# Optimization experiments

Hardware: AMD Instinct MI355X
Metric: run time of the kernel (lower is better)

Reference implementation:

```python
import jax, jax.numpy as jnp
import numpy as np


def setup_inputs() -> dict:
    key = jax.random.key(0)
    k1, k2, k3, k4 = jax.random.split(key, 4)
    T, IN, OUT = 4096, 4096, 4096  # tokens, in_features, out_features
    x = jax.random.normal(k1, (T, IN), dtype=jnp.float32)
    # simulated FP8 weight values (already quantized integers-ish codes stored as float)
    weight = jax.random.normal(k2, (OUT, IN), dtype=jnp.float32)
    # per-output-channel dequant scale
    weight_scale = jax.random.uniform(k3, (OUT,), dtype=jnp.float32, minval=0.01, maxval=0.1)
    bias = jax.random.normal(k4, (OUT,), dtype=jnp.float32)
    return {"x": x, "weight": weight, "weight_scale": weight_scale, "bias": bias}


def reference(x, weight, weight_scale, bias) -> jnp.ndarray:
    # FP8 quantized linear: dequantize weight with per-channel scale, then GEMM + bias.
    # weight: [out, in], weight_scale: [out], x: [tokens, in] -> out: [tokens, out]
    w_deq = weight * weight_scale[:, None]
    return jnp.einsum("ti,oi->to", x, w_deq) + bias
```

## Files before the change

### kernel.cpp

```cpp
#include <hip/hip_runtime.h>
#include <hip/hip_bf16.h>
#include <stdint.h>

typedef __bf16 bf16_t;
typedef bf16_t bf16x8 __attribute__((ext_vector_type(8)));
typedef float f32x4 __attribute__((ext_vector_type(4)));

#define BM 256
#define BN 256
#define BK 64

__device__ __forceinline__ void gload_lds16(const void* g, void* l) {
  __builtin_amdgcn_global_load_lds(
      (const __attribute__((address_space(1))) uint32_t*)g,
      (__attribute__((address_space(3))) uint32_t*)l, 16, 0, 0);
}

__global__ __launch_bounds__(256) void cvt_x_kernel(
    const float* __restrict__ in, bf16_t* __restrict__ out, int n8) {
  int stride = gridDim.x * blockDim.x;
  for (int i = blockIdx.x * blockDim.x + threadIdx.x; i < n8; i += stride) {
    const f32x4* p = (const f32x4*)in + 2 * (size_t)i;
    f32x4 a = p[0], b = p[1];
    bf16x8 o;
#pragma unroll
    for (int r = 0; r < 4; ++r) { o[r] = (bf16_t)a[r]; o[r + 4] = (bf16_t)b[r]; }
    *((bf16x8*)out + i) = o;
  }
}

__global__ __launch_bounds__(256) void cvt_w_kernel(
    const float* __restrict__ in, const float* __restrict__ scale,
    bf16_t* __restrict__ out, int k8, int n8) {
  int stride = gridDim.x * blockDim.x;
  for (int i = blockIdx.x * blockDim.x + threadIdx.x; i < n8; i += stride) {
    int row = i / k8;
    float s = scale[row];
    const f32x4* p = (const f32x4*)in + 2 * (size_t)i;
    f32x4 a = p[0], b = p[1];
    bf16x8 o;
#pragma unroll
    for (int r = 0; r < 4; ++r) {
      o[r] = (bf16_t)(a[r] * s);
      o[r + 4] = (bf16_t)(b[r] * s);
    }
    *((bf16x8*)out + i) = o;
  }
}

__global__ __launch_bounds__(512, 2) void gemm256(
    const bf16_t* __restrict__ A, const bf16_t* __restrict__ B,
    const float* __restrict__ bias, float* __restrict__ C,
    int M, int N, int K) {
  __shared__ __attribute__((aligned(16))) char lds[131072];

  const int tid = threadIdx.x;
  const int lane = tid & 63;
  const int wave = tid >> 6;
  const int wm = wave >> 2;
  const int wn = wave & 3;

  int nwg = gridDim.x;
  int wg = blockIdx.x;
  if ((nwg & 7) == 0) { int cpx = nwg >> 3; wg = (wg & 7) * cpx + (wg >> 3); }
  const int ntn = N / BN;
  const int tm = wg / ntn;
  const int tn = wg % ntn;

  const size_t Kb = (size_t)K * 2;
  const char* gApan = (const char*)A + (size_t)tm * BM * Kb;
  const char* gBpan = (const char*)B + (size_t)tn * BN * Kb;

  const int xc = (((lane >> 4) ^ (lane & 3)) << 4);
  int aoff[2][4], boff[4];
#pragma unroll
  for (int ch = 0; ch < 2; ++ch)
#pragma unroll
    for (int i = 0; i < 4; ++i) {
      int row = wm * 128 + ch * 64 + i * 16 + (lane & 15);
      aoff[ch][i] = row * 64 + xc;
    }
#pragma unroll
  for (int j = 0; j < 4; ++j) {
    int row = wn * 64 + j * 16 + (lane & 15);
    boff[j] = row * 64 + xc;
  }

  size_t srcoff[2];
  int ldst[2];
#pragma unroll
  for (int s = 0; s < 2; ++s) {
    int r = (wave * 2 + s) * 16 + (lane >> 2);
    int c = (lane & 3) ^ (r & 3);
    srcoff[s] = (size_t)r * Kb + (size_t)(c << 4);
    ldst[s] = (wave * 2 + s) * 1024;
  }

#define STAGE_U(dstbase, pan, kbyte)                                          \
  {                                                                           \
    gload_lds16((pan) + srcoff[0] + (size_t)(kbyte), lds + (dstbase) + ldst[0]); \
    gload_lds16((pan) + srcoff[1] + (size_t)(kbyte), lds + (dstbase) + ldst[1]); \
  }

  f32x4 acc[8][4];
#pragma unroll
  for (int a = 0; a < 8; ++a)
#pragma unroll
    for (int j = 0; j < 4; ++j) acc[a][j] = (f32x4)0.0f;

  const int NT = K / BK;

  STAGE_U(0,             gApan, 0);
  STAGE_U(32768,         gBpan, 0);
  STAGE_U(16384,         gApan, 64);
  STAGE_U(49152,         gBpan, 64);
  if (NT > 1) {
    STAGE_U(65536,         gApan, 128);
    STAGE_U(65536 + 32768, gBpan, 128);
    asm volatile("s_waitcnt vmcnt(4)" ::: "memory");
  } else {
    asm volatile("s_waitcnt vmcnt(0)" ::: "memory");
  }
  __builtin_amdgcn_s_barrier();

  for (int t = 0; t < NT; ++t) {
    const int bb = (t & 1) << 16;
    const int nb = bb ^ 65536;
    const size_t kb1 = (size_t)(t + 1) * 128;
    const size_t kb2 = (size_t)(t + 2) * 128;
    const bool st1 = (t + 1) < NT;
    const bool st2 = (t + 2) < NT;

    const char* lA0 = lds + bb;
    const char* lA1 = lds + bb + 16384;
    const char* lB0 = lds + bb + 32768;
    const char* lB1 = lds + bb + 49152;

    bf16x8 af[4], bf0[4], bf1[4];

#pragma unroll
    for (int i = 0; i < 4; ++i) af[i] = *(const bf16x8*)(lA0 + aoff[0][i]);
#pragma unroll
    for (int j = 0; j < 4; ++j) bf0[j] = *(const bf16x8*)(lB0 + boff[j]);
    if (st1) STAGE_U(nb + 16384, gApan, kb1 + 64);
    __builtin_amdgcn_s_barrier();
    asm volatile("s_waitcnt lgkmcnt(0)" ::: "memory");
    __builtin_amdgcn_s_setprio(1);
#pragma unroll
    for (int i = 0; i < 4; ++i)
#pragma unroll
      for (int j = 0; j < 4; ++j)
        acc[i][j] = __builtin_amdgcn_mfma_f32_16x16x32_bf16(af[i], bf0[j],
                                                            acc[i][j], 0, 0, 0);
    __builtin_amdgcn_s_setprio(0);
    __builtin_amdgcn_s_barrier();

#pragma unroll
    for (int i = 0; i < 4; ++i) af[i] = *(const bf16x8*)(lA0 + aoff[1][i]);
    if (st1) STAGE_U(nb + 49152, gBpan, kb1 + 64);
    __builtin_amdgcn_s_barrier();
    asm volatile("s_waitcnt lgkmcnt(0)" ::: "memory");
    __builtin_amdgcn_s_setprio(1);
#pragma unroll
    for (int i = 0; i < 4; ++i)
#pragma unroll
      for (int j = 0; j < 4; ++j)
        acc[4 + i][j] = __builtin_amdgcn_mfma_f32_16x16x32_bf16(
            af[i], bf0[j], acc[4 + i][j], 0, 0, 0);
    __builtin_amdgcn_s_setprio(0);
    __builtin_amdgcn_s_barrier();

#pragma unroll
    for (int i = 0; i < 4; ++i) af[i] = *(const bf16x8*)(lA1 + aoff[0][i]);
#pragma unroll
    for (int j = 0; j < 4; ++j) bf1[j] = *(const bf16x8*)(lB1 + boff[j]);
    if (st2) STAGE_U(bb, gApan, kb2);
    __builtin_amdgcn_s_barrier();
    asm volatile("s_waitcnt lgkmcnt(0)" ::: "memory");
    __builtin_amdgcn_s_setprio(1);
#pragma unroll
    for (int i = 0; i < 4; ++i)
#pragma unroll
      for (int j = 0; j < 4; ++j)
        acc[i][j] = __builtin_amdgcn_mfma_f32_16x16x32_bf16(af[i], bf1[j],
                                                            acc[i][j], 0, 0, 0);
    __builtin_amdgcn_s_setprio(0);
    __builtin_amdgcn_s_barrier();

#pragma unroll
    for (int i = 0; i < 4; ++i) af[i] = *(const bf16x8*)(lA1 + aoff[1][i]);
    if (st2) STAGE_U(bb + 32768, gBpan, kb2);
    __builtin_amdgcn_s_barrier();
    asm volatile("s_waitcnt lgkmcnt(0)" ::: "memory");
    __builtin_amdgcn_s_setprio(1);
#pragma unroll
    for (int i = 0; i < 4; ++i)
#pragma unroll
      for (int j = 0; j < 4; ++j)
        acc[4 + i][j] = __builtin_amdgcn_mfma_f32_16x16x32_bf16(
            af[i], bf1[j], acc[4 + i][j], 0, 0, 0);
    __builtin_amdgcn_s_setprio(0);
    if (st2)      asm volatile("s_waitcnt vmcnt(4)" ::: "memory");
    else if (st1) asm volatile("s_waitcnt vmcnt(0)" ::: "memory");
    __builtin_amdgcn_s_barrier();
  }
#undef STAGE_U

  const int row0 = tm * BM + wm * 128;
  const int col0 = tn * BN + wn * 64;
#pragma unroll
  for (int j = 0; j < 4; ++j) {
    int c = col0 + j * 16 + (lane & 15);
    float bv = bias[c];
#pragma unroll
    for (int a = 0; a < 8; ++a) {
      int ch = a >> 2, i = a & 3;
      int rbase = row0 + ch * 64 + i * 16 + ((lane >> 4) << 2);
#pragma unroll
      for (int r = 0; r < 4; ++r)
        C[(size_t)(rbase + r) * N + c] = acc[a][j][r] + bv;
    }
  }
}

__global__ void fallback_gemm(const float* __restrict__ x,
                              const float* __restrict__ w,
                              const float* __restrict__ s,
                              const float* __restrict__ b,
                              float* __restrict__ out, int M, int N, int K) {
  int o = blockIdx.x * blockDim.x + threadIdx.x;
  if (o >= M * N) return;
  int m = o / N, n = o % N;
  const float* xr = x + (size_t)m * K;
  const float* wr = w + (size_t)n * K;
  float acc = 0.f;
  for (int k = 0; k < K; ++k) acc += xr[k] * wr[k];
  out[o] = acc * s[n] + b[n];
}

extern "C" void kernel_launch(void* const* d_in, const int* in_sizes, int n_in,
                              void* d_out, int out_size, void* d_ws,
                              size_t ws_size, hipStream_t stream) {
  const float* x = (const float*)d_in[0];
  const float* w = (const float*)d_in[1];
  const float* sc = (const float*)d_in[2];
  const float* bias = (const float*)d_in[3];
  float* out = (float*)d_out;

  const int N = in_sizes[2];
  const int K = in_sizes[1] / N;
  const int M = in_sizes[0] / K;

  const size_t need = ((size_t)M * K + (size_t)N * K) * sizeof(bf16_t);
  const bool fast = (ws_size >= need) && (M % BM == 0) && (N % BN == 0) &&
                    (K % BK == 0) && (K / BK >= 1);

  if (fast) {
    bf16_t* xb = (bf16_t*)d_ws;
    bf16_t* wb = xb + (size_t)M * K;

    int n8x = (M * K) / 8;
    int n8w = (N * K) / 8;
    cvt_x_kernel<<<2048, 256, 0, stream>>>(x, xb, n8x);
    cvt_w_kernel<<<2048, 256, 0, stream>>>(w, sc, wb, K / 8, n8w);

    dim3 grid((M / BM) * (N / BN));
    gemm256<<<grid, 512, 0, stream>>>(xb, wb, bias, out, M, N, K);
  } else {
    int total = M * N;
    fallback_gemm<<<(total + 255) / 256, 256, 0, stream>>>(x, w, sc, bias, out,
                                                           M, N, K);
  }
}
```

Measured before the change: 167.5 us.

## Merge conversion kernels into one launch and change LDS swizzle pattern

Fuses the x and weight fp32-to-bf16 conversion kernels into a single launch, with block ranges split between the two jobs, removing one kernel launch and the gap between launches. It also changes the XOR swizzle used for LDS tile layout, both the global-to-LDS write column permutation and the matching read offsets, aiming to reduce LDS bank conflicts on the MFMA operand reads. The swizzle must stay consistent between writer and reader, so a mismatch would corrupt results.

```diff
diff --git a/kernel.cpp b/kernel.cpp
--- a/kernel.cpp
+++ b/kernel.cpp
@@ -16,35 +16,36 @@
       (__attribute__((address_space(3))) uint32_t*)l, 16, 0, 0);
 }
 
-__global__ __launch_bounds__(256) void cvt_x_kernel(
-    const float* __restrict__ in, bf16_t* __restrict__ out, int n8) {
-  int stride = gridDim.x * blockDim.x;
-  for (int i = blockIdx.x * blockDim.x + threadIdx.x; i < n8; i += stride) {
-    const f32x4* p = (const f32x4*)in + 2 * (size_t)i;
-    f32x4 a = p[0], b = p[1];
-    bf16x8 o;
-#pragma unroll
-    for (int r = 0; r < 4; ++r) { o[r] = (bf16_t)a[r]; o[r + 4] = (bf16_t)b[r]; }
-    *((bf16x8*)out + i) = o;
-  }
-}
-
-__global__ __launch_bounds__(256) void cvt_w_kernel(
-    const float* __restrict__ in, const float* __restrict__ scale,
-    bf16_t* __restrict__ out, int k8, int n8) {
-  int stride = gridDim.x * blockDim.x;
-  for (int i = blockIdx.x * blockDim.x + threadIdx.x; i < n8; i += stride) {
-    int row = i / k8;
-    float s = scale[row];
-    const f32x4* p = (const f32x4*)in + 2 * (size_t)i;
-    f32x4 a = p[0], b = p[1];
-    bf16x8 o;
-#pragma unroll
-    for (int r = 0; r < 4; ++r) {
-      o[r] = (bf16_t)(a[r] * s);
-      o[r + 4] = (bf16_t)(b[r] * s);
-    }
-    *((bf16x8*)out + i) = o;
+__global__ __launch_bounds__(256) void cvt_kernel(
+    const float* __restrict__ x, bf16_t* __restrict__ xo, int n8x,
+    const float* __restrict__ w, const float* __restrict__ scale,
+    bf16_t* __restrict__ wo, int k8, int n8w, int gx) {
+  if ((int)blockIdx.x < gx) {
+    int stride = gx * blockDim.x;
+    for (int i = blockIdx.x * blockDim.x + threadIdx.x; i < n8x; i += stride) {
+      const f32x4* p = (const f32x4*)x + 2 * (size_t)i;
+      f32x4 a = p[0], b = p[1];
+      bf16x8 o;
+#pragma unroll
+      for (int r = 0; r < 4; ++r) { o[r] = (bf16_t)a[r]; o[r + 4] = (bf16_t)b[r]; }
+      *((bf16x8*)xo + i) = o;
+    }
+  } else {
+    int stride = (gridDim.x - gx) * blockDim.x;
+    for (int i = (blockIdx.x - gx) * blockDim.x + threadIdx.x; i < n8w;
+         i += stride) {
+      int row = i / k8;
+      float s = scale[row];
+      const f32x4* p = (const f32x4*)w + 2 * (size_t)i;
+      f32x4 a = p[0], b = p[1];
+      bf16x8 o;
+#pragma unroll
+      for (int r = 0; r < 4; ++r) {
+        o[r] = (bf16_t)(a[r] * s);
+        o[r + 4] = (bf16_t)(b[r] * s);
+      }
+      *((bf16x8*)wo + i) = o;
+    }
   }
 }
 
@@ -71,7 +72,7 @@
   const char* gApan = (const char*)A + (size_t)tm * BM * Kb;
   const char* gBpan = (const char*)B + (size_t)tn * BN * Kb;
 
-  const int xc = (((lane >> 4) ^ (lane & 3)) << 4);
+  const int xc = (((lane >> 4) ^ ((lane >> 1) & 3)) << 4);
   int aoff[2][4], boff[4];
 #pragma unroll
   for (int ch = 0; ch < 2; ++ch)
@@ -91,7 +92,7 @@
 #pragma unroll
   for (int s = 0; s < 2; ++s) {
     int r = (wave * 2 + s) * 16 + (lane >> 2);
-    int c = (lane & 3) ^ (r & 3);
+    int c = (lane & 3) ^ ((lane >> 3) & 3);
     srcoff[s] = (size_t)r * Kb + (size_t)(c << 4);
     ldst[s] = (wave * 2 + s) * 1024;
   }
@@ -261,8 +262,9 @@
 
     int n8x = (M * K) / 8;
     int n8w = (N * K) / 8;
-    cvt_x_kernel<<<2048, 256, 0, stream>>>(x, xb, n8x);
-    cvt_w_kernel<<<2048, 256, 0, stream>>>(w, sc, wb, K / 8, n8w);
+    const int gx = 2048;
+    cvt_kernel<<<gx + 2048, 256, 0, stream>>>(x, xb, n8x, w, sc, wb, K / 8,
+                                              n8w, gx);
 
     dim3 grid((M / BM) * (N / BN));
     gemm256<<<grid, 512, 0, stream>>>(xb, wb, bias, out, M, N, K);
```

Measured after the change: 159.6 us. 1.05x faster.
